# Optimization experiments

Hardware: AMD Instinct MI355X
Metric: run time of the kernel (lower is better)

The kernel has to match this reference:

```python
import jax, jax.numpy as jnp
import numpy as np
from math import sqrt

D = 64
HEADS = 8
SEQ = 4096


def setup_inputs() -> dict:
    key = jax.random.key(0)
    ks = jax.random.split(key, 11)
    d, h = D, HEADS
    scale = 1.0 / sqrt(d)
    inp = {
        "q": jax.random.normal(ks[0], (SEQ, d), dtype=jnp.float32),
        "k": jax.random.normal(ks[1], (SEQ, d), dtype=jnp.float32),
        "v": jax.random.normal(ks[2], (SEQ, d), dtype=jnp.float32),
        # Linear(d, d*heads) weights stored as [in, out]; biases [out]
        "qw_w": jax.random.normal(ks[3], (d, d * h), dtype=jnp.float32) * scale,
        "qw_b": jax.random.normal(ks[4], (d * h,), dtype=jnp.float32) * 0.01,
        "kw_w": jax.random.normal(ks[5], (d, d * h), dtype=jnp.float32) * scale,
        "kw_b": jax.random.normal(ks[6], (d * h,), dtype=jnp.float32) * 0.01,
        "vw_w": jax.random.normal(ks[7], (d, d * h), dtype=jnp.float32) * scale,
        "vw_b": jax.random.normal(ks[8], (d * h,), dtype=jnp.float32) * 0.01,
        "ow_w": jax.random.normal(ks[9], (d * h, d), dtype=jnp.float32) * (1.0 / sqrt(d * h)),
        "ow_b": jax.random.normal(ks[10], (d,), dtype=jnp.float32) * 0.01,
    }
    return inp


def reference(q, k, v, qw_w, qw_b, kw_w, kw_b, vw_w, vw_b, ow_w, ow_b):
    d, h = D, HEADS
    # Project: [S, d] @ [d, d*h] -> [S, d*h], then raw reshape to [h, S, d]
    # (matches torch .view(heads, -1, d) on the contiguous projection)
    qh = (q @ qw_w + qw_b).reshape(h, -1, d)
    kh = (k @ kw_w + kw_b).reshape(h, -1, d)
    vh = (v @ vw_w + vw_b).reshape(h, -1, d)
    # scores: [h, S, S]
    scores = jnp.einsum("hqd,hkd->hqk", qh, kh) / sqrt(d)
    attn = jax.nn.softmax(scores, axis=-1)
    ctx = jnp.einsum("hqk,hkd->hqd", attn, vh)  # [h, S, d]
    ctx = ctx.reshape(-1, h * d)  # row-major reshape, matches torch .reshape
    return ctx @ ow_w + ow_b  # [S, d]
```

## Files before the change

kernel.cpp:

```cpp
#include <hip/hip_runtime.h>
#include <stdint.h>

#define SEQL 4096
#define NHEAD 8
#define DHEAD 64
#define HEADELEMS (SEQL * DHEAD)
#define KVBLK 64

typedef unsigned short u16;
typedef __bf16 bf16x8 __attribute__((ext_vector_type(8)));
typedef float f32x16 __attribute__((ext_vector_type(16)));

extern "C" __device__ float __ocml_native_exp2_f32(float);

__device__ __forceinline__ u16 f2bf(float f) {
  union { float f; uint32_t u; } x; x.f = f;
  uint32_t r = x.u + 0x7fffu + ((x.u >> 16) & 1u);
  return (u16)(r >> 16);
}

__device__ __forceinline__ uint32_t cvt_pk_bf16(float lo, float hi) {
  uint32_t r;
  asm("v_cvt_pk_bf16_f32 %0, %1, %2" : "=v"(r) : "v"(lo), "v"(hi));
  return r;
}

__device__ __forceinline__ void pl32_swap(uint32_t& dst, uint32_t& src) {
  asm("v_permlane32_swap_b32 %0, %1" : "+v"(dst), "+v"(src));
}

__device__ __forceinline__ bf16x8 pack_paf(const float* e8) {
  uint32_t w0 = cvt_pk_bf16(e8[0], e8[1]);
  uint32_t w1 = cvt_pk_bf16(e8[2], e8[3]);
  uint32_t w2 = cvt_pk_bf16(e8[4], e8[5]);
  uint32_t w3 = cvt_pk_bf16(e8[6], e8[7]);
  pl32_swap(w0, w2);
  pl32_swap(w1, w3);
  union { uint32_t u[4]; bf16x8 v; } pw;
  pw.u[0] = w0; pw.u[1] = w1; pw.u[2] = w2; pw.u[3] = w3;
  return pw.v;
}

#define GLDS16(g, l)                                                            \
  __builtin_amdgcn_global_load_lds(                                             \
      (const __attribute__((address_space(1))) uint32_t*)(g),                   \
      (__attribute__((address_space(3))) uint32_t*)(l), 16, 0, 0)

__global__ __launch_bounds__(256) void proj_kernel(
    const float* __restrict__ q, const float* __restrict__ k, const float* __restrict__ v,
    const float* __restrict__ qw, const float* __restrict__ qb,
    const float* __restrict__ kw, const float* __restrict__ kb,
    const float* __restrict__ vw, const float* __restrict__ vb,
    u16* __restrict__ Qp, u16* __restrict__ Kp, u16* __restrict__ vhT) {
  const float* X; const float* W; const float* B; float scale;
  if (blockIdx.y == 0)      { X = q; W = qw; B = qb; scale = 0.125f * 1.44269504089f; }
  else if (blockIdx.y == 1) { X = k; W = kw; B = kb; scale = 1.0f; }
  else                      { X = v; W = vw; B = vb; scale = 1.0f; }

  __shared__ float xs[16][64];
  __shared__ __align__(16) u16 vtile[64][136];
  const int t = threadIdx.x;
  const int rowbase = blockIdx.x * 16;
  for (int i = t; i < 16 * 64; i += 256) xs[i >> 6][i & 63] = X[rowbase * 64 + i];
  __syncthreads();

  const int c0 = t * 2;
  float acc0[16] = {}, acc1[16] = {};
  for (int kk = 0; kk < 64; ++kk) {
    const float2 w = *(const float2*)(W + kk * 512 + c0);
    #pragma unroll
    for (int r = 0; r < 16; ++r) {
      const float x = xs[r][kk];
      acc0[r] = fmaf(x, w.x, acc0[r]);
      acc1[r] = fmaf(x, w.y, acc1[r]);
    }
  }
  const float b0 = B[c0], b1 = B[c0 + 1];

  if (blockIdx.y != 2) {
    u16* __restrict__ P = (blockIdx.y == 0) ? Qp : Kp;
    #pragma unroll
    for (int r = 0; r < 16; ++r) {
      const u16 o0 = f2bf((acc0[r] + b0) * scale);
      const u16 o1 = f2bf((acc1[r] + b1) * scale);
      *(uint32_t*)(P + (rowbase + r) * 512 + c0) = ((uint32_t)o1 << 16) | (uint32_t)o0;
    }
  } else {
    const int dd = c0 & 63, cg = c0 >> 6;
    #pragma unroll
    for (int r = 0; r < 16; ++r) {
      vtile[dd][r * 8 + cg]     = f2bf(acc0[r] + b0);
      vtile[dd + 1][r * 8 + cg] = f2bf(acc1[r] + b1);
    }
    __syncthreads();
    const int h = rowbase >> 9;
    const int ibase = (rowbase & 511) * 8;
    u16* __restrict__ dst = vhT + h * HEADELEMS;
    #pragma unroll
    for (int rep = 0; rep < 4; ++rep) {
      const int n = t + rep * 256;
      const int d2 = n >> 4, m = n & 15;
      *(uint4*)(dst + d2 * 4096 + ibase + m * 8) = *(const uint4*)(&vtile[d2][m * 8]);
    }
  }
}

template <int SPLIT>
__global__ __launch_bounds__(256, 2) void attn_kernel(
    const u16* __restrict__ Qp, const u16* __restrict__ Kp,
    const u16* __restrict__ vhT, float* __restrict__ cxp, float* __restrict__ lsp) {
  constexpr int TPQ = 64 / SPLIT;
  const int h = blockIdx.x & 7, idx = blockIdx.x >> 3;
  const int qb = idx / SPLIT, part = idx % SPLIT;
  const int t = threadIdx.x, lane = t & 63;
  const int l32 = lane & 31, hi = lane >> 5;

  __shared__ __align__(16) char smem[3 * 16384 + 32768];
  char* const qlds = smem + 49152;

  const u16* __restrict__ Qh = Qp + h * HEADELEMS;
  const u16* __restrict__ Kh = Kp + h * HEADELEMS;
  const u16* __restrict__ VTh = vhT + h * HEADELEMS;

  int koff[2], voff[2];
  #pragma unroll
  for (int i = 0; i < 2; ++i) {
    const int n = t + i * 256;
    const int r = n >> 3, c = (n & 7) ^ (r & 7);
    koff[i] = r * 64 + c * 8;
    voff[i] = r * 4096 + c * 8;
  }
  const int wuni = (t & 192) * 16;

#define STAGE(j, slot)                                                         \
  {                                                                            \
    const int kb_ = (part * TPQ + (j)) * KVBLK;                                \
    GLDS16(Kh + kb_ * 64 + koff[0], (slot));                                   \
    GLDS16(Kh + kb_ * 64 + koff[1], (slot) + 4096);                            \
    GLDS16(VTh + kb_ + voff[0], (slot) + 8192);                                \
    GLDS16(VTh + kb_ + voff[1], (slot) + 12288);                               \
  }

  {
    const u16* __restrict__ qsrc = Qh + qb * 256 * 64;
    #pragma unroll
    for (int i = 0; i < 8; ++i) {
      const int n = t + i * 256;
      GLDS16(qsrc + (n >> 3) * 64 + (n & 7) * 8, qlds + i * 4096 + wuni);
    }
  }
  __builtin_amdgcn_sched_barrier(0);
  STAGE(0, smem + wuni);
  __builtin_amdgcn_sched_barrier(0);
  STAGE(1, smem + 16384 + wuni);
  __builtin_amdgcn_sched_barrier(0);

  asm volatile("s_waitcnt vmcnt(8)" ::: "memory");
  __builtin_amdgcn_s_barrier();
  __builtin_amdgcn_sched_barrier(0);

  const int qrlA = (t >> 6) * 64 + l32;
  bf16x8 qfA[4], qfB[4];
  #pragma unroll
  for (int ks = 0; ks < 4; ++ks) {
    qfA[ks] = *(const bf16x8*)(qlds + qrlA * 128 + ks * 32 + hi * 16);
    qfB[ks] = *(const bf16x8*)(qlds + (qrlA + 32) * 128 + ks * 32 + hi * 16);
  }

  const f32x16 z16 = {0,0,0,0,0,0,0,0,0,0,0,0,0,0,0,0};
  f32x16 caA0 = z16, caA1 = z16, caB0 = z16, caB1 = z16;
  float lsA[4] = {0.f, 0.f, 0.f, 0.f}, lsB[4] = {0.f, 0.f, 0.f, 0.f};

  for (int it = 0; it < TPQ; ++it) {
    if (it < TPQ - 1) asm volatile("s_waitcnt vmcnt(4) lgkmcnt(0)" ::: "memory");
    else              asm volatile("s_waitcnt vmcnt(0) lgkmcnt(0)" ::: "memory");
    __builtin_amdgcn_s_barrier();
    __builtin_amdgcn_sched_barrier(0);

    char* const cb = smem + (it % 3) * 16384;
    if (it + 2 < TPQ) STAGE(it + 2, smem + ((it + 2) % 3) * 16384 + wuni);
    __builtin_amdgcn_sched_barrier(0);

    f32x16 sA0 = z16, sA1 = z16, sB0 = z16, sB1 = z16;
    const int ar0 = l32, ar1 = l32 + 32;
    __builtin_amdgcn_s_setprio(1);
    #pragma unroll
    for (int ks = 0; ks < 4; ++ks) {
      const int c = ks * 2 + hi;
      const bf16x8 k0 = *(const bf16x8*)(cb + ar0 * 128 + ((c ^ (ar0 & 7)) * 16));
      const bf16x8 k1 = *(const bf16x8*)(cb + ar1 * 128 + ((c ^ (ar1 & 7)) * 16));
      sA0 = __builtin_amdgcn_mfma_f32_32x32x16_bf16(k0, qfA[ks], sA0, 0, 0, 0);
      sA1 = __builtin_amdgcn_mfma_f32_32x32x16_bf16(k1, qfA[ks], sA1, 0, 0, 0);
      sB0 = __builtin_amdgcn_mfma_f32_32x32x16_bf16(k0, qfB[ks], sB0, 0, 0, 0);
      sB1 = __builtin_amdgcn_mfma_f32_32x32x16_bf16(k1, qfB[ks], sB1, 0, 0, 0);
    }
    __builtin_amdgcn_s_setprio(0);

    bf16x8 pafA[4], pafB[4];
    {
      float e[32];
      #pragma unroll
      for (int r = 0; r < 16; ++r) { e[r] = __ocml_native_exp2_f32(sA0[r]); lsA[r & 3] += e[r]; }
      #pragma unroll
      for (int r = 0; r < 16; ++r) { e[16 + r] = __ocml_native_exp2_f32(sA1[r]); lsA[r & 3] += e[16 + r]; }
      #pragma unroll
      for (int ksl = 0; ksl < 4; ++ksl) pafA[ksl] = pack_paf(e + ksl * 8);
    }
    {
      float e[32];
      #pragma unroll
      for (int r = 0; r < 16; ++r) { e[r] = __ocml_native_exp2_f32(sB0[r]); lsB[r & 3] += e[r]; }
      #pragma unroll
      for (int r = 0; r < 16; ++r) { e[16 + r] = __ocml_native_exp2_f32(sB1[r]); lsB[r & 3] += e[16 + r]; }
      #pragma unroll
      for (int ksl = 0; ksl < 4; ++ksl) pafB[ksl] = pack_paf(e + ksl * 8);
    }

    #pragma unroll
    for (int ksl = 0; ksl < 4; ++ksl) {
      const int cl = ksl * 2 + hi;
      const int vr0 = l32, vr1 = l32 + 32;
      const bf16x8 v0 = *(const bf16x8*)(cb + 8192 + vr0 * 128 + ((cl ^ (vr0 & 7)) * 16));
      const bf16x8 v1 = *(const bf16x8*)(cb + 8192 + vr1 * 128 + ((cl ^ (vr1 & 7)) * 16));
      __builtin_amdgcn_s_setprio(1);
      caA0 = __builtin_amdgcn_mfma_f32_32x32x16_bf16(pafA[ksl], v0, caA0, 0, 0, 0);
      caA1 = __builtin_amdgcn_mfma_f32_32x32x16_bf16(pafA[ksl], v1, caA1, 0, 0, 0);
      caB0 = __builtin_amdgcn_mfma_f32_32x32x16_bf16(pafB[ksl], v0, caB0, 0, 0, 0);
      caB1 = __builtin_amdgcn_mfma_f32_32x32x16_bf16(pafB[ksl], v1, caB1, 0, 0, 0);
      __builtin_amdgcn_s_setprio(0);
    }
  }
#undef STAGE

  float lsumA = (lsA[0] + lsA[1]) + (lsA[2] + lsA[3]);
  float lsumB = (lsB[0] + lsB[1]) + (lsB[2] + lsB[3]);
  lsumA += __shfl_xor(lsumA, 32);
  lsumB += __shfl_xor(lsumB, 32);
  const int q0 = qb * 256 + (t >> 6) * 64;
  float* __restrict__ ch = cxp + (part * NHEAD + h) * HEADELEMS;
  #pragma unroll
  for (int reg = 0; reg < 16; ++reg) {
    const int crw = (reg & 3) + 8 * (reg >> 2) + 4 * hi;
    ch[(q0 + crw) * 64 + l32]           = caA0[reg];
    ch[(q0 + crw) * 64 + 32 + l32]      = caA1[reg];
    ch[(q0 + 32 + crw) * 64 + l32]      = caB0[reg];
    ch[(q0 + 32 + crw) * 64 + 32 + l32] = caB1[reg];
  }
  if (hi == 0) {
    lsp[(part * NHEAD + h) * SEQL + q0 + l32]      = lsumA;
    lsp[(part * NHEAD + h) * SEQL + q0 + 32 + l32] = lsumB;
  }
}

template <int SPLIT>
__global__ __launch_bounds__(256) void outproj_kernel(
    const float* __restrict__ cxp, const float* __restrict__ lsp,
    const float* __restrict__ W, const float* __restrict__ B,
    float* __restrict__ out) {
  const int t = threadIdx.x;
  const int r0 = blockIdx.x * 8;
  const int hh = r0 >> 9;
  const int sb0 = (r0 & 511) * 8;

  __shared__ float cn[64][64];
  __shared__ float invs[64];

  if (t < 64) {
    float s = 0.f;
    #pragma unroll
    for (int p = 0; p < SPLIT; ++p) s += lsp[(p * NHEAD + hh) * SEQL + sb0 + t];
    invs[t] = 1.0f / s;
  }
  __syncthreads();

  #pragma unroll
  for (int i = 0; i < 4; ++i) {
    const int n = (t + i * 256) * 4;
    const int s = n >> 6;
    const int base = hh * HEADELEMS + sb0 * 64 + n;
    float4 av = *(const float4*)(cxp + base);
    #pragma unroll
    for (int p = 1; p < SPLIT; ++p) {
      const float4 bv = *(const float4*)(cxp + p * NHEAD * HEADELEMS + base);
      av.x += bv.x; av.y += bv.y; av.z += bv.z; av.w += bv.w;
    }
    const float inv = invs[s];
    av.x *= inv; av.y *= inv; av.z *= inv; av.w *= inv;
    *(float4*)(&cn[s][n & 63]) = av;
  }
  __syncthreads();

  const int col = t & 63;
  const int lr = (t >> 6) * 2;
  float acc0 = 0.f, acc1 = 0.f;
  #pragma unroll 8
  for (int kk = 0; kk < 512; ++kk) {
    const float wv = W[kk * 64 + col];
    acc0 = fmaf(cn[lr * 8 + (kk >> 6)][kk & 63], wv, acc0);
    acc1 = fmaf(cn[lr * 8 + 8 + (kk >> 6)][kk & 63], wv, acc1);
  }
  const float b = B[col];
  out[(r0 + lr) * 64 + col] = acc0 + b;
  out[(r0 + lr + 1) * 64 + col] = acc1 + b;
}

extern "C" void kernel_launch(void* const* d_in, const int* in_sizes, int n_in,
                              void* d_out, int out_size, void* d_ws, size_t ws_size,
                              hipStream_t stream) {
  const float* q  = (const float*)d_in[0];
  const float* k  = (const float*)d_in[1];
  const float* v  = (const float*)d_in[2];
  const float* qw = (const float*)d_in[3];
  const float* qb = (const float*)d_in[4];
  const float* kw = (const float*)d_in[5];
  const float* kb = (const float*)d_in[6];
  const float* vw = (const float*)d_in[7];
  const float* vb = (const float*)d_in[8];
  const float* ow = (const float*)d_in[9];
  const float* ob = (const float*)d_in[10];

  char* ws = (char*)d_ws;
  u16* Qp    = (u16*)(ws);
  u16* Kp    = (u16*)(ws + (4u << 20));
  u16* vhT   = (u16*)(ws + (8u << 20));
  float* cxp = (float*)(ws + (12u << 20));
  float* out = (float*)d_out;

  proj_kernel<<<dim3(SEQL / 16, 3), 256, 0, stream>>>(q, k, v, qw, qb, kw, kb, vw, vb,
                                                      Qp, Kp, vhT);

  const size_t need4 = (12u << 20) + 4u * ((8u << 20) + NHEAD * SEQL * 4u);
  if (ws_size >= need4) {
    float* lsp = (float*)(ws + (12u << 20) + 4u * (8u << 20));
    attn_kernel<4><<<16 * 4 * 8, 256, 0, stream>>>(Qp, Kp, vhT, cxp, lsp);
    outproj_kernel<4><<<SEQL / 8, 256, 0, stream>>>(cxp, lsp, ow, ob, out);
  } else {
    float* lsp = (float*)(ws + (12u << 20) + 2u * (8u << 20));
    attn_kernel<2><<<16 * 2 * 8, 256, 0, stream>>>(Qp, Kp, vhT, cxp, lsp);
    outproj_kernel<2><<<SEQL / 8, 256, 0, stream>>>(cxp, lsp, ow, ob, out);
  }
}
```

Measured before the change: 89.21 us.

## Raise attention KV split to six and load Q directly to registers

Attention now splits each query block's KV range into six parts instead of four, using uneven tile ranges (ts..te), so 768 workgroups are launched. The Q staging through LDS is dropped in favour of direct global loads into registers, which cuts the LDS footprint to three K/V buffers. Launch bounds go up to three workgroups per SIMD. The goal is better occupancy and load balance across the MI355X CUs, at the cost of more partial results for the output-projection reduction to merge and tighter register limits.

```diff
diff --git a/kernel.cpp b/kernel.cpp
--- a/kernel.cpp
+++ b/kernel.cpp
@@ -106,17 +106,17 @@
 }
 
 template <int SPLIT>
-__global__ __launch_bounds__(256, 2) void attn_kernel(
+__global__ __launch_bounds__(256, 3) void attn_kernel(
     const u16* __restrict__ Qp, const u16* __restrict__ Kp,
     const u16* __restrict__ vhT, float* __restrict__ cxp, float* __restrict__ lsp) {
-  constexpr int TPQ = 64 / SPLIT;
   const int h = blockIdx.x & 7, idx = blockIdx.x >> 3;
   const int qb = idx / SPLIT, part = idx % SPLIT;
   const int t = threadIdx.x, lane = t & 63;
   const int l32 = lane & 31, hi = lane >> 5;
-
-  __shared__ __align__(16) char smem[3 * 16384 + 32768];
-  char* const qlds = smem + 49152;
+  const int ts = (part * 64) / SPLIT;
+  const int te = ((part + 1) * 64) / SPLIT;
+
+  __shared__ __align__(16) char smem[3 * 16384];
 
   const u16* __restrict__ Qh = Qp + h * HEADELEMS;
   const u16* __restrict__ Kh = Kp + h * HEADELEMS;
@@ -134,51 +134,39 @@
 
 #define STAGE(j, slot)                                                         \
   {                                                                            \
-    const int kb_ = (part * TPQ + (j)) * KVBLK;                                \
+    const int kb_ = (j) * KVBLK;                                               \
     GLDS16(Kh + kb_ * 64 + koff[0], (slot));                                   \
     GLDS16(Kh + kb_ * 64 + koff[1], (slot) + 4096);                            \
     GLDS16(VTh + kb_ + voff[0], (slot) + 8192);                                \
     GLDS16(VTh + kb_ + voff[1], (slot) + 12288);                               \
   }
 
-  {
-    const u16* __restrict__ qsrc = Qh + qb * 256 * 64;
-    #pragma unroll
-    for (int i = 0; i < 8; ++i) {
-      const int n = t + i * 256;
-      GLDS16(qsrc + (n >> 3) * 64 + (n & 7) * 8, qlds + i * 4096 + wuni);
-    }
-  }
-  __builtin_amdgcn_sched_barrier(0);
-  STAGE(0, smem + wuni);
-  __builtin_amdgcn_sched_barrier(0);
-  STAGE(1, smem + 16384 + wuni);
-  __builtin_amdgcn_sched_barrier(0);
-
-  asm volatile("s_waitcnt vmcnt(8)" ::: "memory");
-  __builtin_amdgcn_s_barrier();
-  __builtin_amdgcn_sched_barrier(0);
-
-  const int qrlA = (t >> 6) * 64 + l32;
+  const int qrow = qb * 256 + (t >> 6) * 64 + l32;
   bf16x8 qfA[4], qfB[4];
   #pragma unroll
   for (int ks = 0; ks < 4; ++ks) {
-    qfA[ks] = *(const bf16x8*)(qlds + qrlA * 128 + ks * 32 + hi * 16);
-    qfB[ks] = *(const bf16x8*)(qlds + (qrlA + 32) * 128 + ks * 32 + hi * 16);
-  }
+    qfA[ks] = *(const bf16x8*)(Qh + qrow * 64 + ks * 16 + hi * 8);
+    qfB[ks] = *(const bf16x8*)(Qh + (qrow + 32) * 64 + ks * 16 + hi * 8);
+  }
+  __builtin_amdgcn_sched_barrier(0);
+
+  STAGE(ts, smem + wuni);
+  __builtin_amdgcn_sched_barrier(0);
+  STAGE(ts + 1, smem + 16384 + wuni);
+  __builtin_amdgcn_sched_barrier(0);
 
   const f32x16 z16 = {0,0,0,0,0,0,0,0,0,0,0,0,0,0,0,0};
   f32x16 caA0 = z16, caA1 = z16, caB0 = z16, caB1 = z16;
   float lsA[4] = {0.f, 0.f, 0.f, 0.f}, lsB[4] = {0.f, 0.f, 0.f, 0.f};
 
-  for (int it = 0; it < TPQ; ++it) {
-    if (it < TPQ - 1) asm volatile("s_waitcnt vmcnt(4) lgkmcnt(0)" ::: "memory");
-    else              asm volatile("s_waitcnt vmcnt(0) lgkmcnt(0)" ::: "memory");
+  for (int it = ts; it < te; ++it) {
+    if (it < te - 1) asm volatile("s_waitcnt vmcnt(4) lgkmcnt(0)" ::: "memory");
+    else             asm volatile("s_waitcnt vmcnt(0) lgkmcnt(0)" ::: "memory");
     __builtin_amdgcn_s_barrier();
     __builtin_amdgcn_sched_barrier(0);
 
-    char* const cb = smem + (it % 3) * 16384;
-    if (it + 2 < TPQ) STAGE(it + 2, smem + ((it + 2) % 3) * 16384 + wuni);
+    char* const cb = smem + ((it - ts) % 3) * 16384;
+    if (it + 2 < te) STAGE(it + 2, smem + ((it - ts + 2) % 3) * 16384 + wuni);
     __builtin_amdgcn_sched_barrier(0);
 
     f32x16 sA0 = z16, sA1 = z16, sB0 = z16, sB1 = z16;
@@ -329,14 +317,14 @@
   proj_kernel<<<dim3(SEQL / 16, 3), 256, 0, stream>>>(q, k, v, qw, qb, kw, kb, vw, vb,
                                                       Qp, Kp, vhT);
 
-  const size_t need4 = (12u << 20) + 4u * ((8u << 20) + NHEAD * SEQL * 4u);
-  if (ws_size >= need4) {
+  const size_t need6 = (12u << 20) + 6u * ((8u << 20) + NHEAD * SEQL * 4u);
+  if (ws_size >= need6) {
+    float* lsp = (float*)(ws + (12u << 20) + 6u * (8u << 20));
+    attn_kernel<6><<<16 * 8 * 6, 256, 0, stream>>>(Qp, Kp, vhT, cxp, lsp);
+    outproj_kernel<6><<<SEQL / 8, 256, 0, stream>>>(cxp, lsp, ow, ob, out);
+  } else {
     float* lsp = (float*)(ws + (12u << 20) + 4u * (8u << 20));
-    attn_kernel<4><<<16 * 4 * 8, 256, 0, stream>>>(Qp, Kp, vhT, cxp, lsp);
+    attn_kernel<4><<<16 * 8 * 4, 256, 0, stream>>>(Qp, Kp, vhT, cxp, lsp);
     outproj_kernel<4><<<SEQL / 8, 256, 0, stream>>>(cxp, lsp, ow, ob, out);
-  } else {
-    float* lsp = (float*)(ws + (12u << 20) + 2u * (8u << 20));
-    attn_kernel<2><<<16 * 2 * 8, 256, 0, stream>>>(Qp, Kp, vhT, cxp, lsp);
-    outproj_kernel<2><<<SEQL / 8, 256, 0, stream>>>(cxp, lsp, ow, ob, out);
-  }
-}
+  }
+}
```

New measurement: 206.4 us. 131% more time.
